# Kernel optimization log

Hardware: AMD Instinct MI355X
Metric: run time of the kernel (lower is better)

The kernel has to match this reference:

```python
import jax, jax.numpy as jnp
import numpy as np

INPUT_DIM, HIDDEN, HEADS = 310, 64, 8
WINDOW, PERIOD = 5, 3
NEG_INF = -jnp.inf


def _masks(seq_len):
    i = jnp.arange(seq_len)[:, None]
    j = jnp.arange(seq_len)[None, :]
    local = jnp.abs(i - j) <= WINDOW
    sparse = (j % PERIOD == 0) | (i == j)
    to_add = lambda m: jnp.where(m, 0.0, NEG_INF).astype(jnp.float32)
    return to_add(local), to_add(sparse)


def _mha(xp, in_w, in_b, out_w, out_b, mask):
    # xp: [B,S,E]; in_w: [3E,E]; out_w: [E,E]; mask: [S,S] additive
    B, S, E = xp.shape
    d = E // HEADS
    qkv = xp @ in_w.T + in_b                      # [B,S,3E]
    q, k, v = jnp.split(qkv, 3, axis=-1)
    split_heads = lambda t: t.reshape(B, S, HEADS, d).transpose(0, 2, 1, 3)
    q, k, v = split_heads(q), split_heads(k), split_heads(v)
    scores = jnp.einsum('bhqd,bhkd->bhqk', q, k) / jnp.sqrt(jnp.float32(d))
    scores = scores + mask                         # broadcast [S,S]
    attn = jax.nn.softmax(scores, axis=-1)
    o = jnp.einsum('bhqk,bhkd->bhqd', attn, v)
    o = o.transpose(0, 2, 1, 3).reshape(B, S, E)
    return o @ out_w.T + out_b


def setup_inputs() -> dict:
    key = jax.random.key(0)
    ks = jax.random.split(key, 16)
    E = HIDDEN
    s = lambda fan: 1.0 / np.sqrt(fan)
    u = lambda k, shape, fan: jax.random.uniform(k, shape, jnp.float32, -s(fan), s(fan))
    return {
        'x': jax.random.normal(ks[0], (16, 1024, INPUT_DIM), jnp.float32),
        'proj_w': u(ks[1], (E, INPUT_DIM), INPUT_DIM),
        'proj_b': u(ks[2], (E,), INPUT_DIM),
        'loc_in_w': u(ks[3], (3 * E, E), E),
        'loc_in_b': jnp.zeros((3 * E,), jnp.float32),
        'loc_out_w': u(ks[4], (E, E), E),
        'loc_out_b': jnp.zeros((E,), jnp.float32),
        'glob_in_w': u(ks[5], (3 * E, E), E),
        'glob_in_b': jnp.zeros((3 * E,), jnp.float32),
        'glob_out_w': u(ks[6], (E, E), E),
        'glob_out_b': jnp.zeros((E,), jnp.float32),
        'fusion_w': u(ks[7], (E, 2 * E), 2 * E),
        'fusion_b': u(ks[8], (E,), 2 * E),
        'pool_w1': u(ks[9], (E // 2, E), E),
        'pool_b1': u(ks[10], (E // 2,), E),
        'pool_w2': u(ks[11], (1, E // 2), E // 2),
        'pool_b2': u(ks[12], (1,), E // 2),
    }


def reference(x, proj_w, proj_b, loc_in_w, loc_in_b, loc_out_w, loc_out_b,
              glob_in_w, glob_in_b, glob_out_w, glob_out_b,
              fusion_w, fusion_b, pool_w1, pool_b1, pool_w2, pool_b2):
    B, S, _ = x.shape
    local_mask, sparse_mask = _masks(S)
    xp = x @ proj_w.T + proj_b                     # [B,S,E]
    local_out = _mha(xp, loc_in_w, loc_in_b, loc_out_w, loc_out_b, local_mask)
    global_out = _mha(xp, glob_in_w, glob_in_b, glob_out_w, glob_out_b, sparse_mask)
    fused = jnp.concatenate([local_out, global_out], axis=-1) @ fusion_w.T + fusion_b
    scores = jnp.tanh(fused @ pool_w1.T + pool_b1) @ pool_w2.T + pool_b2  # [B,S,1]
    w = jax.nn.softmax(scores, axis=1)             # softmax over seq dim
    return jnp.sum(fused * w, axis=1)              # [B,E]
```

## Files before the change

### kernel.cpp

```cpp
#include <hip/hip_runtime.h>


typedef __attribute__((ext_vector_type(8))) short short8;
typedef __attribute__((ext_vector_type(4))) float float4v;

#define INV_SQRT8 0.3535533905932738f

__device__ __forceinline__ float4 ld4(const float* p) { return *(const float4*)p; }

__device__ __forceinline__ float4 f4fma(float s, float4 w, float4 a) {
  a.x = fmaf(s, w.x, a.x); a.y = fmaf(s, w.y, a.y);
  a.z = fmaf(s, w.z, a.z); a.w = fmaf(s, w.w, a.w);
  return a;
}

__device__ __forceinline__ void bsplit(float x, short& h, short& l) {
  unsigned xb = __float_as_uint(x);
  unsigned hb = (xb + 0x7fffu + ((xb >> 16) & 1u)) & 0xffff0000u;
  h = (short)(hb >> 16);
  float lf = x - __uint_as_float(hb);
  unsigned lb = __float_as_uint(lf);
  l = (short)((lb + 0x7fffu + ((lb >> 16) & 1u)) >> 16);
}

__global__ __launch_bounds__(256) void prep_w(
    const float* __restrict__ pw, const float* __restrict__ liw,
    const float* __restrict__ giw, const float* __restrict__ fw,
    const float* __restrict__ low, const float* __restrict__ gow,
    const float* __restrict__ lob, const float* __restrict__ gob,
    const float* __restrict__ fb,
    short* __restrict__ wb, float* __restrict__ bc, float* __restrict__ numden)
{
  unsigned idx = blockIdx.x * 256 + threadIdx.x;
  float v; unsigned ho, lo_;
  if (idx < 20480u) {
    unsigned r = idx / 320u, k = idx - r * 320u;
    v = (k < 310u) ? pw[r * 310u + k] : 0.f;
    ho = 0u + idx; lo_ = 20480u + idx;
  } else if (idx < 32768u) {
    unsigned i = idx - 20480u; v = liw[i]; ho = 40960u + i; lo_ = 53248u + i;
  } else if (idx < 45056u) {
    unsigned i = idx - 32768u; v = giw[i]; ho = 65536u + i; lo_ = 77824u + i;
  } else {
    unsigned i = idx - 45056u;
    unsigned n = i >> 7, k = i & 127u;
    float s = 0.f;
    if (k < 64u) {
      for (int e = 0; e < 64; e++) s += fw[n * 128 + e] * low[e * 64 + k];
    } else {
      for (int e = 0; e < 64; e++) s += fw[n * 128 + 64 + e] * gow[e * 64 + (k - 64u)];
    }
    v = s; ho = 90112u + i; lo_ = 98304u + i;
  }
  short h, l; bsplit(v, h, l);
  wb[ho] = h; wb[lo_] = l;
  if (idx < 64u) {
    float b = fb[idx];
    for (int e = 0; e < 64; e++)
      b += lob[e] * fw[idx * 128 + e] + gob[e] * fw[idx * 128 + 64 + e];
    bc[idx] = b;
  }
  if (idx < 1040u) numden[idx] = 0.f;
}

__global__ __launch_bounds__(256) void gemm_proj(
    const float* __restrict__ X,
    const short* __restrict__ Wh, const short* __restrict__ Wl,
    const float* __restrict__ bias,
    short* __restrict__ Ch, short* __restrict__ Cl)
{
  const int lane = threadIdx.x & 63;
  const int w = threadIdx.x >> 6;
  const int q = lane >> 4, r = lane & 15;
  const int m0 = blockIdx.x * 64 + w * 16;
  const int n0 = blockIdx.y * 32;

  float bv0 = bias[n0 + r], bv1 = bias[n0 + 16 + r];
  float4v acc0 = {bv0, bv0, bv0, bv0};
  float4v acc1 = {bv1, bv1, bv1, bv1};

  const float* arow = X + (size_t)(m0 + r) * 310;

  #pragma unroll
  for (int ks = 0; ks < 10; ks++) {
    const int k0 = ks * 32 + q * 8;
    float av[8];
    if (ks < 9) {
      const float* ap = arow + k0;
      #pragma unroll
      for (int t = 0; t < 4; t++) {
        float2 f = *(const float2*)(ap + t * 2);
        av[t*2] = f.x; av[t*2+1] = f.y;
      }
    } else {
      #pragma unroll
      for (int j = 0; j < 8; j++) {
        int kidx = k0 + j;
        av[j] = (kidx < 310) ? arow[kidx] : 0.f;
      }
    }
    short8 ah, al;
    #pragma unroll
    for (int i = 0; i < 8; i++) { short h, l; bsplit(av[i], h, l); ah[i]=h; al[i]=l; }
    short8 bh0 = *(const short8*)(Wh + (size_t)(n0 + r) * 320 + k0);
    short8 bl0 = *(const short8*)(Wl + (size_t)(n0 + r) * 320 + k0);
    short8 bh1 = *(const short8*)(Wh + (size_t)(n0 + 16 + r) * 320 + k0);
    short8 bl1 = *(const short8*)(Wl + (size_t)(n0 + 16 + r) * 320 + k0);
    acc0 = __builtin_amdgcn_mfma_f32_16x16x32_bf16(al, bh0, acc0, 0, 0, 0);
    acc0 = __builtin_amdgcn_mfma_f32_16x16x32_bf16(ah, bl0, acc0, 0, 0, 0);
    acc0 = __builtin_amdgcn_mfma_f32_16x16x32_bf16(ah, bh0, acc0, 0, 0, 0);
    acc1 = __builtin_amdgcn_mfma_f32_16x16x32_bf16(al, bh1, acc1, 0, 0, 0);
    acc1 = __builtin_amdgcn_mfma_f32_16x16x32_bf16(ah, bl1, acc1, 0, 0, 0);
    acc1 = __builtin_amdgcn_mfma_f32_16x16x32_bf16(ah, bh1, acc1, 0, 0, 0);
  }

  #pragma unroll
  for (int e = 0; e < 4; e++) {
    const int row = m0 + q * 4 + e;
    short h, l;
    bsplit(acc0[e], h, l);
    Ch[(size_t)row * 64 + n0 + r] = h; Cl[(size_t)row * 64 + n0 + r] = l;
    bsplit(acc1[e], h, l);
    Ch[(size_t)row * 64 + n0 + 16 + r] = h; Cl[(size_t)row * 64 + n0 + 16 + r] = l;
  }
}

template<int KP>
__global__ __launch_bounds__(256) void gemm_mfma(
    const short* __restrict__ Ah, const short* __restrict__ Al,
    const short* __restrict__ Wh0, const short* __restrict__ Wl0,
    const short* __restrict__ Wh1, const short* __restrict__ Wl1,
    const float* __restrict__ bias0, const float* __restrict__ bias1,
    float* __restrict__ C0, float* __restrict__ C1, int ldc)
{
  const int z = blockIdx.z;
  const short* Wh = z ? Wh1 : Wh0;
  const short* Wl = z ? Wl1 : Wl0;
  const float* bias = z ? bias1 : bias0;
  float* C = z ? C1 : C0;

  const int lane = threadIdx.x & 63;
  const int w = threadIdx.x >> 6;
  const int q = lane >> 4, r = lane & 15;
  const int m0 = blockIdx.x * 64 + w * 16;
  const int n0 = blockIdx.y * 32;

  float bv0 = bias[n0 + r], bv1 = bias[n0 + 16 + r];
  float4v acc0 = {bv0, bv0, bv0, bv0};
  float4v acc1 = {bv1, bv1, bv1, bv1};

  #pragma unroll
  for (int ks = 0; ks < KP / 32; ks++) {
    const int k0 = ks * 32 + q * 8;
    short8 ah = *(const short8*)(Ah + (size_t)(m0 + r) * KP + k0);
    short8 al = *(const short8*)(Al + (size_t)(m0 + r) * KP + k0);
    short8 bh0 = *(const short8*)(Wh + (size_t)(n0 + r) * KP + k0);
    short8 bl0 = *(const short8*)(Wl + (size_t)(n0 + r) * KP + k0);
    short8 bh1 = *(const short8*)(Wh + (size_t)(n0 + 16 + r) * KP + k0);
    short8 bl1 = *(const short8*)(Wl + (size_t)(n0 + 16 + r) * KP + k0);
    acc0 = __builtin_amdgcn_mfma_f32_16x16x32_bf16(al, bh0, acc0, 0, 0, 0);
    acc0 = __builtin_amdgcn_mfma_f32_16x16x32_bf16(ah, bl0, acc0, 0, 0, 0);
    acc0 = __builtin_amdgcn_mfma_f32_16x16x32_bf16(ah, bh0, acc0, 0, 0, 0);
    acc1 = __builtin_amdgcn_mfma_f32_16x16x32_bf16(al, bh1, acc1, 0, 0, 0);
    acc1 = __builtin_amdgcn_mfma_f32_16x16x32_bf16(ah, bl1, acc1, 0, 0, 0);
    acc1 = __builtin_amdgcn_mfma_f32_16x16x32_bf16(ah, bh1, acc1, 0, 0, 0);
  }

  #pragma unroll
  for (int e = 0; e < 4; e++) {
    const int row = m0 + q * 4 + e;
    C[(size_t)row * ldc + n0 + r] = acc0[e];
    C[(size_t)row * ldc + n0 + 16 + r] = acc1[e];
  }
}

__global__ __launch_bounds__(256) void prep_kv(
    const float* __restrict__ qkv,
    short* __restrict__ KH, short* __restrict__ KL,
    short* __restrict__ VTh, short* __restrict__ VTl)
{
  unsigned idx = blockIdx.x * 256 + threadIdx.x;
  if (idx < 360448u) {
    unsigned bh = idx / 2816u;
    unsigned rem = idx - bh * 2816u;
    unsigned kk = rem >> 3, d = rem & 7u;
    float v = (kk < 342u)
      ? qkv[((size_t)((bh >> 3) * 1024 + kk * 3)) * 192 + 64 + (bh & 7u) * 8 + d]
      : 0.f;
    short h, l; bsplit(v, h, l);
    KH[idx] = h; KL[idx] = l;
  } else {
    unsigned j = idx - 360448u;
    unsigned bh = j / 5632u;
    unsigned rem = j - bh * 5632u;
    unsigned n = rem / 352u, kk = rem - n * 352u;
    float v;
    if (n < 8u) {
      v = (kk < 342u)
        ? qkv[((size_t)((bh >> 3) * 1024 + kk * 3)) * 192 + 128 + (bh & 7u) * 8 + n]
        : 0.f;
    } else {
      v = (n == 8u) ? 1.f : 0.f;
    }
    short h, l; bsplit(v, h, l);
    VTh[j] = h; VTl[j] = l;
  }
}

__global__ __launch_bounds__(256) void mfma_gattn(
    const float* __restrict__ qkv,
    const short* __restrict__ KH, const short* __restrict__ KL,
    const short* __restrict__ VTh, const short* __restrict__ VTl,
    float* __restrict__ o_g, float* __restrict__ pl)
{
  __shared__ short Pbuf[4][2][2][16][32];
  const int b = blockIdx.x, h = blockIdx.y, qt = blockIdx.z;
  const int w = threadIdx.x >> 6, lane = threadIdx.x & 63;
  const int quad = lane >> 4, r = lane & 15;
  const int bh = b * 8 + h;
  const int m0 = qt * 64 + w * 16;

  const short8 z8 = {0,0,0,0,0,0,0,0};
  short8 qh = z8, ql = z8;
  if (quad == 0) {
    const float* qp = qkv + (size_t)(b * 1024 + m0 + r) * 192 + h * 8;
    #pragma unroll
    for (int d = 0; d < 8; d++) { short hh, ll; bsplit(qp[d], hh, ll); qh[d]=hh; ql[d]=ll; }
  }
  const short* kbase  = KH + (size_t)bh * 2816;
  const short* klbase = KL + (size_t)bh * 2816;
  const short* vhbase = VTh + ((size_t)bh * 16 + r) * 352;
  const short* vlbase = VTl + ((size_t)bh * 16 + r) * 352;

  float4v oacc = {0.f, 0.f, 0.f, 0.f};

  for (int kc = 0; kc < 11; kc++) {
    short8 kh0 = z8, kl0 = z8, kh1 = z8, kl1 = z8;
    if (quad == 0) {
      kh0 = *(const short8*)(kbase  + (size_t)(kc * 32 + r) * 8);
      kl0 = *(const short8*)(klbase + (size_t)(kc * 32 + r) * 8);
      kh1 = *(const short8*)(kbase  + (size_t)(kc * 32 + 16 + r) * 8);
      kl1 = *(const short8*)(klbase + (size_t)(kc * 32 + 16 + r) * 8);
    }
    float4v s0 = {0.f,0.f,0.f,0.f}, s1 = {0.f,0.f,0.f,0.f};
    s0 = __builtin_amdgcn_mfma_f32_16x16x32_bf16(qh, kl0, s0, 0, 0, 0);
    s0 = __builtin_amdgcn_mfma_f32_16x16x32_bf16(ql, kh0, s0, 0, 0, 0);
    s0 = __builtin_amdgcn_mfma_f32_16x16x32_bf16(qh, kh0, s0, 0, 0, 0);
    s1 = __builtin_amdgcn_mfma_f32_16x16x32_bf16(qh, kl1, s1, 0, 0, 0);
    s1 = __builtin_amdgcn_mfma_f32_16x16x32_bf16(ql, kh1, s1, 0, 0, 0);
    s1 = __builtin_amdgcn_mfma_f32_16x16x32_bf16(qh, kh1, s1, 0, 0, 0);

    const int par = kc & 1;
    const int key0 = kc * 32 + r, key1 = key0 + 16;
    #pragma unroll
    for (int e = 0; e < 4; e++) {
      float p0 = (key0 < 342) ? __expf(s0[e] * INV_SQRT8) : 0.f;
      float p1 = (key1 < 342) ? __expf(s1[e] * INV_SQRT8) : 0.f;
      short h0, l0, h1, l1; bsplit(p0, h0, l0); bsplit(p1, h1, l1);
      const int qloc = quad * 4 + e;
      Pbuf[w][par][0][qloc][r]      = h0;
      Pbuf[w][par][0][qloc][16 + r] = h1;
      Pbuf[w][par][1][qloc][r]      = l0;
      Pbuf[w][par][1][qloc][16 + r] = l1;
    }
    short8 pA = *(const short8*)&Pbuf[w][par][0][r][quad * 8];
    short8 pB = *(const short8*)&Pbuf[w][par][1][r][quad * 8];
    short8 vh = *(const short8*)(vhbase + kc * 32 + quad * 8);
    short8 vl = *(const short8*)(vlbase + kc * 32 + quad * 8);
    oacc = __builtin_amdgcn_mfma_f32_16x16x32_bf16(pA, vl, oacc, 0, 0, 0);
    oacc = __builtin_amdgcn_mfma_f32_16x16x32_bf16(pB, vh, oacc, 0, 0, 0);
    oacc = __builtin_amdgcn_mfma_f32_16x16x32_bf16(pA, vh, oacc, 0, 0, 0);
  }

  #pragma unroll
  for (int e = 0; e < 4; e++) {
    const int orow = b * 1024 + m0 + quad * 4 + e;
    if (r < 8)       o_g[(size_t)orow * 64 + h * 8 + r] = oacc[e];
    else if (r == 8) pl[(size_t)orow * 8 + h] = oacc[e];
  }
}

__global__ __launch_bounds__(256) void local_attn(
    const float* __restrict__ qkv, float* __restrict__ o)
{
  int t = blockIdx.x * 256 + threadIdx.x;
  int h = t & 7;
  int i = (t >> 3) & 1023;
  int b = t >> 13;
  const float* base = qkv + (size_t)b * 1024 * 192;
  const float* qp = base + (size_t)i * 192 + h * 8;
  float4 q0 = ld4(qp), q1 = ld4(qp + 4);
  float l = 0.f;
  float4 o0 = make_float4(0.f, 0.f, 0.f, 0.f);
  float4 o1 = make_float4(0.f, 0.f, 0.f, 0.f);
  int jlo = i - 5; if (jlo < 0) jlo = 0;
  int jhi = i + 5; if (jhi > 1023) jhi = 1023;
  for (int j = jlo; j <= jhi; j++) {
    const float* kp = base + (size_t)j * 192 + 64 + h * 8;
    float4 k0 = ld4(kp), k1 = ld4(kp + 4);
    float s = q0.x * k0.x + q0.y * k0.y + q0.z * k0.z + q0.w * k0.w
            + q1.x * k1.x + q1.y * k1.y + q1.z * k1.z + q1.w * k1.w;
    float p = __expf(s * INV_SQRT8);
    l += p;
    float4 v0 = ld4(kp + 64), v1 = ld4(kp + 68);
    o0 = f4fma(p, v0, o0);
    o1 = f4fma(p, v1, o1);
  }
  float inv = 1.f / l;
  float* op = o + (size_t)(b * 1024 + i) * 64 + h * 8;
  float4 r0, r1;
  r0.x = o0.x * inv; r0.y = o0.y * inv; r0.z = o0.z * inv; r0.w = o0.w * inv;
  r1.x = o1.x * inv; r1.y = o1.y * inv; r1.z = o1.z * inv; r1.w = o1.w * inv;
  *(float4*)op = r0;
  *(float4*)(op + 4) = r1;
}

__global__ __launch_bounds__(256) void gemm_fuse(
    const float* __restrict__ o_l, const float* __restrict__ o_g,
    const float* __restrict__ pl, const float* __restrict__ qkv_g,
    const short* __restrict__ Wh, const short* __restrict__ Wl,
    const float* __restrict__ bc, float* __restrict__ C)
{
  const int lane = threadIdx.x & 63;
  const int w = threadIdx.x >> 6;
  const int q = lane >> 4, r = lane & 15;
  const int m0 = blockIdx.x * 64 + w * 16;
  const int n0 = blockIdx.y * 32;

  float bv0 = bc[n0 + r], bv1 = bc[n0 + 16 + r];
  float4v acc0 = {bv0, bv0, bv0, bv0};
  float4v acc1 = {bv1, bv1, bv1, bv1};

  #pragma unroll
  for (int ks = 0; ks < 4; ks++) {
    const int k0 = ks * 32 + q * 8;
    const int row = m0 + r;
    float av[8];
    if (ks < 2) {
      const float* ap = o_l + (size_t)row * 64 + k0;
      float4 f0 = ld4(ap), f1 = ld4(ap + 4);
      av[0]=f0.x; av[1]=f0.y; av[2]=f0.z; av[3]=f0.w;
      av[4]=f1.x; av[5]=f1.y; av[6]=f1.z; av[7]=f1.w;
    } else {
      const int off = k0 - 64;
      const int h = off >> 3;
      const float* op = o_g + (size_t)row * 64 + off;
      float4 O0 = ld4(op), O1 = ld4(op + 4);
      float l = pl[(size_t)row * 8 + h];
      const int i = row & 1023;
      if (i % 3 != 0) {
        const float* base = qkv_g + (size_t)row * 192;
        const float* qp = base + h * 8;
        const float* kp = base + 64 + h * 8;
        const float* vp = base + 128 + h * 8;
        float4 q0 = ld4(qp), q1 = ld4(qp + 4);
        float4 k0v = ld4(kp), k1v = ld4(kp + 4);
        float s = q0.x*k0v.x + q0.y*k0v.y + q0.z*k0v.z + q0.w*k0v.w
                + q1.x*k1v.x + q1.y*k1v.y + q1.z*k1v.z + q1.w*k1v.w;
        float p = __expf(s * INV_SQRT8);
        float4 v0 = ld4(vp), v1 = ld4(vp + 4);
        O0 = f4fma(p, v0, O0); O1 = f4fma(p, v1, O1);
        l += p;
      }
      float inv = 1.f / l;
      av[0]=O0.x*inv; av[1]=O0.y*inv; av[2]=O0.z*inv; av[3]=O0.w*inv;
      av[4]=O1.x*inv; av[5]=O1.y*inv; av[6]=O1.z*inv; av[7]=O1.w*inv;
    }
    short8 ah, al;
    #pragma unroll
    for (int i2 = 0; i2 < 8; i2++) { short h2, l2; bsplit(av[i2], h2, l2); ah[i2]=h2; al[i2]=l2; }
    short8 bh0 = *(const short8*)(Wh + (size_t)(n0 + r) * 128 + k0);
    short8 bl0 = *(const short8*)(Wl + (size_t)(n0 + r) * 128 + k0);
    short8 bh1 = *(const short8*)(Wh + (size_t)(n0 + 16 + r) * 128 + k0);
    short8 bl1 = *(const short8*)(Wl + (size_t)(n0 + 16 + r) * 128 + k0);
    acc0 = __builtin_amdgcn_mfma_f32_16x16x32_bf16(al, bh0, acc0, 0, 0, 0);
    acc0 = __builtin_amdgcn_mfma_f32_16x16x32_bf16(ah, bl0, acc0, 0, 0, 0);
    acc0 = __builtin_amdgcn_mfma_f32_16x16x32_bf16(ah, bh0, acc0, 0, 0, 0);
    acc1 = __builtin_amdgcn_mfma_f32_16x16x32_bf16(al, bh1, acc1, 0, 0, 0);
    acc1 = __builtin_amdgcn_mfma_f32_16x16x32_bf16(ah, bl1, acc1, 0, 0, 0);
    acc1 = __builtin_amdgcn_mfma_f32_16x16x32_bf16(ah, bh1, acc1, 0, 0, 0);
  }

  #pragma unroll
  for (int e = 0; e < 4; e++) {
    const int row = m0 + q * 4 + e;
    C[(size_t)row * 64 + n0 + r] = acc0[e];
    C[(size_t)row * 64 + n0 + 16 + r] = acc1[e];
  }
}

__global__ __launch_bounds__(256) void score_pool(
    const float* __restrict__ fused,
    const float* __restrict__ pw1, const float* __restrict__ pb1,
    const float* __restrict__ pw2, const float* __restrict__ pb2,
    float* __restrict__ num, float* __restrict__ den)
{
  __shared__ float partial[4][64];
  __shared__ float Ls[64][65];
  const int b = blockIdx.x, c = blockIdx.y;
  const int w = threadIdx.x >> 6, lane = threadIdx.x & 63;
  const int row = b * 1024 + c * 64 + lane;
  const float* f = fused + (size_t)row * 64;
  float4 fr[16];
  #pragma unroll
  for (int e = 0; e < 16; e++) fr[e] = ld4(f + e * 4);

  float psc = 0.f;
  #pragma unroll
  for (int jj = 0; jj < 8; jj++) {
    const int j = w * 8 + jj;
    const float* wr = pw1 + j * 64;
    float hj = pb1[j];
    #pragma unroll
    for (int e = 0; e < 16; e++) {
      float4 wv = ld4(wr + e * 4);
      hj += fr[e].x * wv.x + fr[e].y * wv.y + fr[e].z * wv.z + fr[e].w * wv.w;
    }
    float e2 = __expf(2.f * hj);
    psc += ((e2 - 1.f) / (e2 + 1.f)) * pw2[j];
  }
  partial[w][lane] = psc;
  __syncthreads();
  if (w == 0) {
    float sc = pb2[0] + partial[0][lane] + partial[1][lane]
             + partial[2][lane] + partial[3][lane];
    float p = __expf(sc);
    #pragma unroll
    for (int e = 0; e < 16; e++) {
      Ls[lane][e*4+0] = p * fr[e].x; Ls[lane][e*4+1] = p * fr[e].y;
      Ls[lane][e*4+2] = p * fr[e].z; Ls[lane][e*4+3] = p * fr[e].w;
    }
    float colsum = 0.f;
    #pragma unroll 8
    for (int s = 0; s < 64; s++) colsum += Ls[s][lane];
    atomicAdd(&num[b * 64 + lane], colsum);
    float ps = p;
    #pragma unroll
    for (int off = 32; off > 0; off >>= 1)
      ps += __shfl_xor(ps, off, 64);
    if (lane == 0) atomicAdd(&den[b], ps);
  }
}

__global__ __launch_bounds__(1024) void finalize(
    const float* __restrict__ num, const float* __restrict__ den,
    float* __restrict__ out)
{
  int t = threadIdx.x;
  out[t] = num[t] / den[t >> 6];
}

extern "C" void kernel_launch(void* const* d_in, const int* in_sizes, int n_in,
                              void* d_out, int out_size, void* d_ws, size_t ws_size,
                              hipStream_t stream)
{
  const float* x          = (const float*)d_in[0];
  const float* proj_w     = (const float*)d_in[1];
  const float* proj_b     = (const float*)d_in[2];
  const float* loc_in_w   = (const float*)d_in[3];
  const float* loc_in_b   = (const float*)d_in[4];
  const float* loc_out_w  = (const float*)d_in[5];
  const float* loc_out_b  = (const float*)d_in[6];
  const float* glob_in_w  = (const float*)d_in[7];
  const float* glob_in_b  = (const float*)d_in[8];
  const float* glob_out_w = (const float*)d_in[9];
  const float* glob_out_b = (const float*)d_in[10];
  const float* fusion_w   = (const float*)d_in[11];
  const float* fusion_b   = (const float*)d_in[12];
  const float* pw1        = (const float*)d_in[13];
  const float* pb1        = (const float*)d_in[14];
  const float* pw2        = (const float*)d_in[15];
  const float* pb2        = (const float*)d_in[16];

  float* ws = (float*)d_ws;
  float* qkv_g = ws;
  short* xph   = (short*)(ws + 3538944);
  short* xpl   = (short*)(ws + 4063232);
  float* fused = ws + 3538944;
  float* qkv_l = ws + 4587520;
  float* o_l   = ws + 7733248;
  float* o_g   = ws + 8781824;
  float* pl    = ws + 9830400;
  short* KH    = (short*)(ws + 9961472);
  short* KL    = (short*)(ws + 10141696);
  short* VTh   = (short*)(ws + 10321920);
  short* VTl   = (short*)(ws + 10682368);
  float* bc    = ws + 11042816;
  float* numden= ws + 11042880;
  float* num   = numden;
  float* den   = numden + 1024;
  short* wb    = (short*)(ws + 11043920);
  short* projh = wb;           short* projl = wb + 20480;
  short* linh  = wb + 40960;   short* linl  = wb + 53248;
  short* ginh  = wb + 65536;   short* ginl  = wb + 77824;
  short* wfh   = wb + 90112;   short* wfl   = wb + 98304;
  float* out   = (float*)d_out;

  dim3 blk(256);
  prep_w<<<208, blk, 0, stream>>>(proj_w, loc_in_w, glob_in_w, fusion_w,
                                  loc_out_w, glob_out_w, loc_out_b, glob_out_b,
                                  fusion_b, wb, bc, numden);
  gemm_proj<<<dim3(256, 2), blk, 0, stream>>>(x, projh, projl, proj_b, xph, xpl);
  gemm_mfma<64><<<dim3(256, 6, 2), blk, 0, stream>>>(
      xph, xpl, linh, linl, ginh, ginl, loc_in_b, glob_in_b,
      qkv_l, qkv_g, 192);
  prep_kv<<<4224, blk, 0, stream>>>(qkv_g, KH, KL, VTh, VTl);
  local_attn<<<512, blk, 0, stream>>>(qkv_l, o_l);
  mfma_gattn<<<dim3(16, 8, 16), blk, 0, stream>>>(qkv_g, KH, KL, VTh, VTl, o_g, pl);
  gemm_fuse<<<dim3(256, 2, 1), blk, 0, stream>>>(
      o_l, o_g, pl, qkv_g, wfh, wfl, bc, fused);
  score_pool<<<dim3(16, 16), blk, 0, stream>>>(
      fused, pw1, pb1, pw2, pb2, num, den);
  finalize<<<1, dim3(1024), 0, stream>>>(num, den, out);
}
```

Baseline: 194.4 us.

## Fuse local attention into KV prep and fuse gemm with score pooling

Merges the local attention kernel into the K/V split-prep kernel as extra blocks, and fuses the fusion GEMM with the score/pool kernel so each block computes a full 64x64 output tile, stages it in shared memory, and pools it directly. This removes two launches and the global write and read of the fused tensor. In exchange the fuse GEMM runs half as many blocks, each holding four accumulators, which lowers parallelism, and the Ls shared buffer now uses a padded stride of 68.

```diff
diff --git a/kernel.cpp b/kernel.cpp
--- a/kernel.cpp
+++ b/kernel.cpp
@@ -174,36 +174,71 @@
   }
 }
 
-__global__ __launch_bounds__(256) void prep_kv(
-    const float* __restrict__ qkv,
+__global__ __launch_bounds__(256) void prep_kv_local(
+    const float* __restrict__ qkv_g, const float* __restrict__ qkv_l,
     short* __restrict__ KH, short* __restrict__ KL,
-    short* __restrict__ VTh, short* __restrict__ VTl)
-{
-  unsigned idx = blockIdx.x * 256 + threadIdx.x;
-  if (idx < 360448u) {
-    unsigned bh = idx / 2816u;
-    unsigned rem = idx - bh * 2816u;
-    unsigned kk = rem >> 3, d = rem & 7u;
-    float v = (kk < 342u)
-      ? qkv[((size_t)((bh >> 3) * 1024 + kk * 3)) * 192 + 64 + (bh & 7u) * 8 + d]
-      : 0.f;
-    short h, l; bsplit(v, h, l);
-    KH[idx] = h; KL[idx] = l;
+    short* __restrict__ VTh, short* __restrict__ VTl,
+    float* __restrict__ o_l)
+{
+  const int u = blockIdx.x;
+  if (u < 4224) {
+    unsigned idx = (unsigned)u * 256u + threadIdx.x;
+    if (idx < 360448u) {
+      unsigned bh = idx / 2816u;
+      unsigned rem = idx - bh * 2816u;
+      unsigned kk = rem >> 3, d = rem & 7u;
+      float v = (kk < 342u)
+        ? qkv_g[((size_t)((bh >> 3) * 1024 + kk * 3)) * 192 + 64 + (bh & 7u) * 8 + d]
+        : 0.f;
+      short h, l; bsplit(v, h, l);
+      KH[idx] = h; KL[idx] = l;
+    } else if (idx < 1081344u) {
+      unsigned j = idx - 360448u;
+      unsigned bh = j / 5632u;
+      unsigned rem = j - bh * 5632u;
+      unsigned n = rem / 352u, kk = rem - n * 352u;
+      float v;
+      if (n < 8u) {
+        v = (kk < 342u)
+          ? qkv_g[((size_t)((bh >> 3) * 1024 + kk * 3)) * 192 + 128 + (bh & 7u) * 8 + n]
+          : 0.f;
+      } else {
+        v = (n == 8u) ? 1.f : 0.f;
+      }
+      short h, l; bsplit(v, h, l);
+      VTh[j] = h; VTl[j] = l;
+    }
   } else {
-    unsigned j = idx - 360448u;
-    unsigned bh = j / 5632u;
-    unsigned rem = j - bh * 5632u;
-    unsigned n = rem / 352u, kk = rem - n * 352u;
-    float v;
-    if (n < 8u) {
-      v = (kk < 342u)
-        ? qkv[((size_t)((bh >> 3) * 1024 + kk * 3)) * 192 + 128 + (bh & 7u) * 8 + n]
-        : 0.f;
-    } else {
-      v = (n == 8u) ? 1.f : 0.f;
-    }
-    short h, l; bsplit(v, h, l);
-    VTh[j] = h; VTl[j] = l;
+    int t = (u - 4224) * 256 + threadIdx.x;
+    int h = t & 7;
+    int i = (t >> 3) & 1023;
+    int b = t >> 13;
+    const float* base = qkv_l + (size_t)b * 1024 * 192;
+    const float* qp = base + (size_t)i * 192 + h * 8;
+    float4 q0 = ld4(qp), q1 = ld4(qp + 4);
+    float l = 0.f;
+    float4 o0 = make_float4(0.f, 0.f, 0.f, 0.f);
+    float4 o1 = make_float4(0.f, 0.f, 0.f, 0.f);
+    int jlo = i - 5; if (jlo < 0) jlo = 0;
+    int jhi = i + 5; if (jhi > 1023) jhi = 1023;
+    for (int j = jlo; j <= jhi; j++) {
+      const float* kp = base + (size_t)j * 192 + 64 + h * 8;
+      float4 k0 = ld4(kp), k1 = ld4(kp + 4);
+      float s = q0.x * k0.x + q0.y * k0.y + q0.z * k0.z + q0.w * k0.w
+              + q1.x * k1.x + q1.y * k1.y + q1.z * k1.z + q1.w * k1.w;
+      float p = __expf(s * INV_SQRT8);
+      l += p;
+      float4 v0 = ld4(kp + 64), v1 = ld4(kp + 68);
+      o0 = f4fma(p, v0, o0);
+      o1 = f4fma(p, v1, o1);
+    }
+    float inv = 1.f / l;
+    float* op = o_l + (size_t)(b * 1024 + i) * 64 + h * 8;
+    float4 r0, r1;
+    r0.x = o0.x * inv; r0.y = o0.y * inv; r0.z = o0.z * inv; r0.w = o0.w * inv;
+    r1.x = o1.x * inv; r1.y = o1.y * inv; r1.z = o1.z * inv; r1.w = o1.w * inv;
+    *(float4*)op = r0;
+    *(float4*)(op + 4) = r1;
   }
 }
 
@@ -280,60 +315,34 @@
   }
 }
 
-__global__ __launch_bounds__(256) void local_attn(
-    const float* __restrict__ qkv, float* __restrict__ o)
-{
-  int t = blockIdx.x * 256 + threadIdx.x;
-  int h = t & 7;
-  int i = (t >> 3) & 1023;
-  int b = t >> 13;
-  const float* base = qkv + (size_t)b * 1024 * 192;
-  const float* qp = base + (size_t)i * 192 + h * 8;
-  float4 q0 = ld4(qp), q1 = ld4(qp + 4);
-  float l = 0.f;
-  float4 o0 = make_float4(0.f, 0.f, 0.f, 0.f);
-  float4 o1 = make_float4(0.f, 0.f, 0.f, 0.f);
-  int jlo = i - 5; if (jlo < 0) jlo = 0;
-  int jhi = i + 5; if (jhi > 1023) jhi = 1023;
-  for (int j = jlo; j <= jhi; j++) {
-    const float* kp = base + (size_t)j * 192 + 64 + h * 8;
-    float4 k0 = ld4(kp), k1 = ld4(kp + 4);
-    float s = q0.x * k0.x + q0.y * k0.y + q0.z * k0.z + q0.w * k0.w
-            + q1.x * k1.x + q1.y * k1.y + q1.z * k1.z + q1.w * k1.w;
-    float p = __expf(s * INV_SQRT8);
-    l += p;
-    float4 v0 = ld4(kp + 64), v1 = ld4(kp + 68);
-    o0 = f4fma(p, v0, o0);
-    o1 = f4fma(p, v1, o1);
-  }
-  float inv = 1.f / l;
-  float* op = o + (size_t)(b * 1024 + i) * 64 + h * 8;
-  float4 r0, r1;
-  r0.x = o0.x * inv; r0.y = o0.y * inv; r0.z = o0.z * inv; r0.w = o0.w * inv;
-  r1.x = o1.x * inv; r1.y = o1.y * inv; r1.z = o1.z * inv; r1.w = o1.w * inv;
-  *(float4*)op = r0;
-  *(float4*)(op + 4) = r1;
-}
-
-__global__ __launch_bounds__(256) void gemm_fuse(
+__global__ __launch_bounds__(256) void gemm_fuse_score(
     const float* __restrict__ o_l, const float* __restrict__ o_g,
     const float* __restrict__ pl, const float* __restrict__ qkv_g,
     const short* __restrict__ Wh, const short* __restrict__ Wl,
-    const float* __restrict__ bc, float* __restrict__ C)
-{
-  const int lane = threadIdx.x & 63;
-  const int w = threadIdx.x >> 6;
-  const int q = lane >> 4, r = lane & 15;
-  const int m0 = blockIdx.x * 64 + w * 16;
-  const int n0 = blockIdx.y * 32;
-
-  float bv0 = bc[n0 + r], bv1 = bc[n0 + 16 + r];
-  float4v acc0 = {bv0, bv0, bv0, bv0};
-  float4v acc1 = {bv1, bv1, bv1, bv1};
+    const float* __restrict__ bc,
+    const float* __restrict__ pw1, const float* __restrict__ pb1,
+    const float* __restrict__ pw2, const float* __restrict__ pb2,
+    float* __restrict__ num, float* __restrict__ den)
+{
+  __shared__ float Ls[64][68];
+  __shared__ float partial[4][64];
+  const int tid = threadIdx.x;
+  const int lane = tid & 63, w = tid >> 6;
+  const int quad = lane >> 4, r = lane & 15;
+  const int bx = blockIdx.x;
+  const int m0 = bx * 64 + w * 16;
+
+  float4v acc[4];
+  #pragma unroll
+  for (int g = 0; g < 4; g++) {
+    float bv = bc[g * 16 + r];
+    float4v t = {bv, bv, bv, bv};
+    acc[g] = t;
+  }
 
   #pragma unroll
   for (int ks = 0; ks < 4; ks++) {
-    const int k0 = ks * 32 + q * 8;
+    const int k0 = ks * 32 + quad * 8;
     const int row = m0 + r;
     float av[8];
     if (ks < 2) {
@@ -351,10 +360,10 @@
       if (i % 3 != 0) {
         const float* base = qkv_g + (size_t)row * 192;
         const float* qp = base + h * 8;
-        const float* kp = base + 64 + h * 8;
+        const float* kpp = base + 64 + h * 8;
         const float* vp = base + 128 + h * 8;
         float4 q0 = ld4(qp), q1 = ld4(qp + 4);
-        float4 k0v = ld4(kp), k1v = ld4(kp + 4);
+        float4 k0v = ld4(kpp), k1v = ld4(kpp + 4);
         float s = q0.x*k0v.x + q0.y*k0v.y + q0.z*k0v.z + q0.w*k0v.w
                 + q1.x*k1v.x + q1.y*k1v.y + q1.z*k1v.z + q1.w*k1v.w;
         float p = __expf(s * INV_SQRT8);
@@ -369,41 +378,26 @@
     short8 ah, al;
     #pragma unroll
     for (int i2 = 0; i2 < 8; i2++) { short h2, l2; bsplit(av[i2], h2, l2); ah[i2]=h2; al[i2]=l2; }
-    short8 bh0 = *(const short8*)(Wh + (size_t)(n0 + r) * 128 + k0);
-    short8 bl0 = *(const short8*)(Wl + (size_t)(n0 + r) * 128 + k0);
-    short8 bh1 = *(const short8*)(Wh + (size_t)(n0 + 16 + r) * 128 + k0);
-    short8 bl1 = *(const short8*)(Wl + (size_t)(n0 + 16 + r) * 128 + k0);
-    acc0 = __builtin_amdgcn_mfma_f32_16x16x32_bf16(al, bh0, acc0, 0, 0, 0);
-    acc0 = __builtin_amdgcn_mfma_f32_16x16x32_bf16(ah, bl0, acc0, 0, 0, 0);
-    acc0 = __builtin_amdgcn_mfma_f32_16x16x32_bf16(ah, bh0, acc0, 0, 0, 0);
-    acc1 = __builtin_amdgcn_mfma_f32_16x16x32_bf16(al, bh1, acc1, 0, 0, 0);
-    acc1 = __builtin_amdgcn_mfma_f32_16x16x32_bf16(ah, bl1, acc1, 0, 0, 0);
-    acc1 = __builtin_amdgcn_mfma_f32_16x16x32_bf16(ah, bh1, acc1, 0, 0, 0);
-  }
-
-  #pragma unroll
-  for (int e = 0; e < 4; e++) {
-    const int row = m0 + q * 4 + e;
-    C[(size_t)row * 64 + n0 + r] = acc0[e];
-    C[(size_t)row * 64 + n0 + 16 + r] = acc1[e];
-  }
-}
-
-__global__ __launch_bounds__(256) void score_pool(
-    const float* __restrict__ fused,
-    const float* __restrict__ pw1, const float* __restrict__ pb1,
-    const float* __restrict__ pw2, const float* __restrict__ pb2,
-    float* __restrict__ num, float* __restrict__ den)
-{
-  __shared__ float partial[4][64];
-  __shared__ float Ls[64][65];
-  const int b = blockIdx.x, c = blockIdx.y;
-  const int w = threadIdx.x >> 6, lane = threadIdx.x & 63;
-  const int row = b * 1024 + c * 64 + lane;
-  const float* f = fused + (size_t)row * 64;
+    #pragma unroll
+    for (int g = 0; g < 4; g++) {
+      short8 bh = *(const short8*)(Wh + (size_t)(g * 16 + r) * 128 + k0);
+      short8 bl = *(const short8*)(Wl + (size_t)(g * 16 + r) * 128 + k0);
+      acc[g] = __builtin_amdgcn_mfma_f32_16x16x32_bf16(al, bh, acc[g], 0, 0, 0);
+      acc[g] = __builtin_amdgcn_mfma_f32_16x16x32_bf16(ah, bl, acc[g], 0, 0, 0);
+      acc[g] = __builtin_amdgcn_mfma_f32_16x16x32_bf16(ah, bh, acc[g], 0, 0, 0);
+    }
+  }
+
+  #pragma unroll
+  for (int g = 0; g < 4; g++)
+    #pragma unroll
+    for (int e = 0; e < 4; e++)
+      Ls[w * 16 + quad * 4 + e][g * 16 + r] = acc[g][e];
+  __syncthreads();
+
   float4 fr[16];
   #pragma unroll
-  for (int e = 0; e < 16; e++) fr[e] = ld4(f + e * 4);
+  for (int e = 0; e < 16; e++) fr[e] = *(float4*)&Ls[lane][e * 4];
 
   float psc = 0.f;
   #pragma unroll
@@ -422,6 +416,7 @@
   partial[w][lane] = psc;
   __syncthreads();
   if (w == 0) {
+    const int b = bx >> 4;
     float sc = pb2[0] + partial[0][lane] + partial[1][lane]
              + partial[2][lane] + partial[3][lane];
     float p = __expf(sc);
@@ -476,7 +471,6 @@
   float* qkv_g = ws;
   short* xph   = (short*)(ws + 3538944);
   short* xpl   = (short*)(ws + 4063232);
-  float* fused = ws + 3538944;
   float* qkv_l = ws + 4587520;
   float* o_l   = ws + 7733248;
   float* o_g   = ws + 8781824;
@@ -504,12 +498,9 @@
   gemm_mfma<64><<<dim3(256, 6, 2), blk, 0, stream>>>(
       xph, xpl, linh, linl, ginh, ginl, loc_in_b, glob_in_b,
       qkv_l, qkv_g, 192);
-  prep_kv<<<4224, blk, 0, stream>>>(qkv_g, KH, KL, VTh, VTl);
-  local_attn<<<512, blk, 0, stream>>>(qkv_l, o_l);
+  prep_kv_local<<<4736, blk, 0, stream>>>(qkv_g, qkv_l, KH, KL, VTh, VTl, o_l);
   mfma_gattn<<<dim3(16, 8, 16), blk, 0, stream>>>(qkv_g, KH, KL, VTh, VTl, o_g, pl);
-  gemm_fuse<<<dim3(256, 2, 1), blk, 0, stream>>>(
-      o_l, o_g, pl, qkv_g, wfh, wfl, bc, fused);
-  score_pool<<<dim3(16, 16), blk, 0, stream>>>(
-      fused, pw1, pb1, pw2, pb2, num, den);
+  gemm_fuse_score<<<256, blk, 0, stream>>>(
+      o_l, o_g, pl, qkv_g, wfh, wfl, bc, pw1, pb1, pw2, pb2, num, den);
   finalize<<<1, dim3(1024), 0, stream>>>(num, den, out);
 }
```

Result: no change. 194.0 us (-0.2%).
